# Kernel optimization log

Measured on AMD Instinct MI355X. Metric: run time of the kernel, lower is better.

## Reference

```python
import jax, jax.numpy as jnp
import numpy as np

NUM_CODEBOOKS = 4
COMMITMENT_WEIGHT = 0.25

def setup_inputs() -> dict:
    key = jax.random.key(0)
    k1, k2, k3 = jax.random.split(key, 3)
    B, T, C, K = 16, 2048, 512, 1024
    x = jax.random.normal(k1, (B, T, C), dtype=jnp.float32)
    mask = jax.random.randint(k2, (B, T), 0, 2).astype(jnp.bool_)
    codebooks = jax.random.normal(k3, (NUM_CODEBOOKS, K, C), dtype=jnp.float32) / np.sqrt(C)
    return {"x": x, "mask": mask, "codebooks": codebooks}

def reference(x, mask, codebooks):
    # x: [B,T,C], mask: [B,T] bool, codebooks: [Q,K,C]
    B, T, C = x.shape
    maskf = mask.astype(x.dtype)[..., None]          # [B,T,1]
    n_valid = jnp.maximum(mask.sum().astype(x.dtype), 1.0)
    denom = n_valid * C                               # mse over valid elements
    residual = x
    x_q = jnp.zeros_like(x)
    vq_loss = jnp.zeros((), dtype=x.dtype)
    idx_list = []
    for i in range(NUM_CODEBOOKS):
        cb = codebooks[i]                             # [K,C]
        a2 = jnp.sum(residual * residual, axis=-1, keepdims=True)   # [B,T,1]
        b2 = jnp.sum(cb * cb, axis=-1)                              # [K]
        ab = jnp.einsum('btc,kc->btk', residual, cb)                # [B,T,K]
        dist = a2 + b2 - 2.0 * ab
        idx = jnp.argmin(dist, axis=-1)                             # [B,T]
        q = cb[idx]                                                 # [B,T,C]
        # masked MSE losses (mean over valid elements)
        d1 = (q - jax.lax.stop_gradient(residual)) * maskf
        d2 = (residual - jax.lax.stop_gradient(q)) * maskf
        vq_loss = vq_loss + jnp.sum(d1 * d1) / denom
        vq_loss = vq_loss + COMMITMENT_WEIGHT * jnp.sum(d2 * d2) / denom
        # straight-through, applied only at valid positions
        q_st = residual + jax.lax.stop_gradient(q - residual)
        x_q = x_q + q_st * maskf
        residual = residual - q_st * maskf
        idx_list.append(idx)
    indices = jnp.stack(idx_list, axis=-1)                          # [B,T,Q]
    indices = jnp.where(mask[..., None], indices, -1).astype(jnp.int64)
    x_q = x_q * maskf
    return x_q, indices, vq_loss
```

## Files before the change

kernel.cpp:

```cpp
#include <hip/hip_runtime.h>

#define BT 32768
#define CDIM 512
#define KCB 1024
#define NQ 4
#define IDX_BASE (BT*CDIM)
#define LOSS_OFF (BT*CDIM + BT*NQ)
#define CAND_MAX 64
#define MARGIN_C 0.0025f
#define MARGIN_A 0.004f

#define WS_LIST   256
#define WS_A2     (WS_LIST + BT*4)
#define WS_B2     (WS_A2 + BT*4)
#define WS_RBC    (WS_B2 + NQ*KCB*4)
#define WS_CBB    (WS_RBC + BT*CDIM*2)
#define WS_CCNT   (WS_CBB + NQ*KCB*CDIM*2)
#define WS_CANDK  (WS_CCNT + BT*4)
#define WS_CANDS  (WS_CANDK + BT*CAND_MAX*4)
#define WS_IDXS   (WS_CANDS + BT*CAND_MAX*4)

typedef __attribute__((ext_vector_type(8))) _Float16 f16x8;
typedef __attribute__((ext_vector_type(4))) float f32x4;

__device__ __forceinline__ unsigned int f2h(float f) {
  union { _Float16 h; unsigned short u; } cv;
  cv.h = (_Float16)f;
  return (unsigned int)cv.u;
}

__device__ __forceinline__ int nth_bit(unsigned long long m, int n) {
  int pos = 0;
#pragma unroll
  for (int w = 32; w >= 1; w >>= 1) {
    unsigned long long lowmask = (w == 64) ? ~0ull : ((1ull << w) - 1ull);
    int c = __popcll(m & lowmask);
    if (n >= c) { n -= c; m >>= w; pos += w; }
  }
  return pos;
}

__device__ __forceinline__ float chain512q(const float* lds_r, const float* brow) {
  const float4* b4 = (const float4*)brow;
  float4 cur[8], nxt[8];
#pragma unroll
  for (int q = 0; q < 8; ++q) cur[q] = b4[q];
  float ab = 0.f;
#pragma unroll 1
  for (int seg = 0; seg < 15; ++seg) {
#pragma unroll
    for (int q = 0; q < 8; ++q) nxt[q] = b4[(seg + 1) * 8 + q];
#pragma unroll
    for (int q = 0; q < 8; ++q) {
      float4 bv = cur[q];
      float4 rv = *(const float4*)&lds_r[(seg * 8 + q) * 4];
      ab = __fmaf_rn(rv.x, bv.x, ab);
      ab = __fmaf_rn(rv.y, bv.y, ab);
      ab = __fmaf_rn(rv.z, bv.z, ab);
      ab = __fmaf_rn(rv.w, bv.w, ab);
    }
#pragma unroll
    for (int q = 0; q < 8; ++q) cur[q] = nxt[q];
  }
#pragma unroll
  for (int q = 0; q < 8; ++q) {
    float4 bv = cur[q];
    float4 rv = *(const float4*)&lds_r[(120 + q) * 4];
    ab = __fmaf_rn(rv.x, bv.x, ab);
    ab = __fmaf_rn(rv.y, bv.y, ab);
    ab = __fmaf_rn(rv.z, bv.z, ab);
    ab = __fmaf_rn(rv.w, bv.w, ab);
  }
  return ab;
}

__device__ __forceinline__ int mask_at(const void* m, int t, int flag) {
  switch (flag) {
    case 0:  return ((const unsigned char*)m)[t] != 0;
    case 1:  return ((const int*)m)[t] != 0;
    case 2:  return ((const unsigned long long*)m)[t] != 0ull;
    case 3:  return ((const unsigned short*)m)[t] != 0;
    default: return ((const float*)m)[t] != 0.0f;
  }
}

__global__ void k_prep(const unsigned char* mask, int* wsi, float* wsf, int* list) {
  __shared__ int s_not01, s_off1, s_offn0, s_odd, s_fm;
  __shared__ int s_cnt[1024];
  int tid = threadIdx.x;
  if (tid == 0) { s_not01 = 0; s_off1 = 0; s_offn0 = 0; s_odd = 0; }
  __syncthreads();
  int l_not01 = 0, l_off1 = 0, l_offn0 = 0, l_odd = 0;
  for (int o = tid; o < BT; o += 1024) {
    unsigned char b = mask[o];
    if (b) {
      if (b > 1) l_not01 = 1;
      int m4 = o & 3;
      if (m4 == 1) l_off1 = 1;
      if (m4) l_offn0 = 1;
      if ((o & 7) >= 4) l_odd = 1;
    }
  }
  if (l_not01) atomicOr(&s_not01, 1);
  if (l_off1)  atomicOr(&s_off1, 1);
  if (l_offn0) atomicOr(&s_offn0, 1);
  if (l_odd)   atomicOr(&s_odd, 1);
  __syncthreads();
  if (tid == 0) {
    int fm;
    if (s_not01)      fm = s_off1 ? 3 : 4;
    else if (s_offn0) fm = 0;
    else if (s_odd)   fm = 1;
    else              fm = 2;
    s_fm = fm; wsi[0] = fm;
    wsf[8] = 0.0f;
    wsf[12] = 0.f; wsf[13] = 0.f; wsf[14] = 0.f; wsf[15] = 0.f;
  }
  __syncthreads();
  int fm = s_fm;
  int base = tid * 32, cnt = 0;
  for (int u = 0; u < 32; u++) cnt += mask_at(mask, base + u, fm);
  int val = cnt;
  s_cnt[tid] = val;
  __syncthreads();
#pragma unroll
  for (int off = 1; off < 1024; off <<= 1) {
    int v = (tid >= off) ? s_cnt[tid - off] : 0;
    __syncthreads();
    val += v;
    s_cnt[tid] = val;
    __syncthreads();
  }
  if (tid == 0) wsi[2] = s_cnt[1023];
  int woff = val - cnt;
  for (int u = 0; u < 32; u++) {
    int t = base + u;
    if (mask_at(mask, t, fm)) list[woff++] = t;
  }
}

__global__ void k_fill(const void* mask, float* out, const int* wsi) {
  int w = threadIdx.x >> 6, lane = threadIdx.x & 63;
  int t = blockIdx.x * 4 + w;
  if (t >= BT) return;
  if (mask_at(mask, t, wsi[0])) return;
  float4 z = make_float4(0.f, 0.f, 0.f, 0.f);
  float4* p = (float4*)(out + (size_t)t * CDIM) + lane * 2;
  p[0] = z; p[1] = z;
  if (lane < NQ) out[IDX_BASE + (size_t)t * NQ + lane] = -1.0f;
}

__global__ void k_b2(const float* __restrict__ cb, float* __restrict__ b2, float* b2max) {
  __shared__ float st[4][512];
  int w = threadIdx.x >> 6, lane = threadIdx.x & 63;
  int row = blockIdx.x * 4 + w;
  const float4* p = (const float4*)(cb + (size_t)row * CDIM) + lane * 2;
  float4 v0 = p[0], v1 = p[1];
  *(float4*)&st[w][lane * 8] = v0;
  *(float4*)&st[w][lane * 8 + 4] = v1;
  __syncthreads();
  if (threadIdx.x < 4) {
    int r2 = blockIdx.x * 4 + threadIdx.x;
    float s = 0.f;
    for (int c4 = 0; c4 < 128; ++c4) {
      float4 v = *(float4*)&st[threadIdx.x][c4 * 4];
      s = __fadd_rn(s, __fmul_rn(v.x, v.x));
      s = __fadd_rn(s, __fmul_rn(v.y, v.y));
      s = __fadd_rn(s, __fmul_rn(v.z, v.z));
      s = __fadd_rn(s, __fmul_rn(v.w, v.w));
    }
    b2[r2] = s;
    atomicMax((int*)&b2max[r2 >> 10], __float_as_int(s));
  }
}

__global__ void k_cvtcb(const float* __restrict__ cb, unsigned short* __restrict__ cbb) {
  size_t i = (size_t)blockIdx.x * blockDim.x + threadIdx.x;
  const float4* s = (const float4*)(cb + i * 8);
  float4 a = s[0], b = s[1];
  uint4 u;
  u.x = f2h(a.x) | (f2h(a.y) << 16);
  u.y = f2h(a.z) | (f2h(a.w) << 16);
  u.z = f2h(b.x) | (f2h(b.y) << 16);
  u.w = f2h(b.z) | (f2h(b.w) << 16);
  *(uint4*)(cbb + i * 8) = u;
}

__global__ __launch_bounds__(256) void k_init(const float* __restrict__ x,
    float* __restrict__ rws, unsigned short* __restrict__ rbc,
    const int* __restrict__ wsi, const int* __restrict__ list,
    float* __restrict__ a2c, int* __restrict__ candcnt) {
  __shared__ float st[8][512];
  int nv = wsi[2];
  int j0 = blockIdx.x * 8;
  int tid = threadIdx.x;
  if (tid < 8) candcnt[j0 + tid] = 0;
  if (j0 >= nv) return;
  int slot = tid >> 5;
  int j = j0 + slot;
  int c0 = (tid & 31) * 16;
  if (j < nv) {
    int t = list[j];
    const float4* src = (const float4*)(x + (size_t)t * CDIM + c0);
    float4* dst = (float4*)(rws + (size_t)t * CDIM + c0);
    float4 v0 = src[0], v1 = src[1], v2 = src[2], v3 = src[3];
    dst[0] = v0; dst[1] = v1; dst[2] = v2; dst[3] = v3;
    *(float4*)&st[slot][c0]      = v0; *(float4*)&st[slot][c0 + 4]  = v1;
    *(float4*)&st[slot][c0 + 8]  = v2; *(float4*)&st[slot][c0 + 12] = v3;
    uint4 u0, u1;
    u0.x = f2h(v0.x) | (f2h(v0.y) << 16); u0.y = f2h(v0.z) | (f2h(v0.w) << 16);
    u0.z = f2h(v1.x) | (f2h(v1.y) << 16); u0.w = f2h(v1.z) | (f2h(v1.w) << 16);
    u1.x = f2h(v2.x) | (f2h(v2.y) << 16); u1.y = f2h(v2.z) | (f2h(v2.w) << 16);
    u1.z = f2h(v3.x) | (f2h(v3.y) << 16); u1.w = f2h(v3.z) | (f2h(v3.w) << 16);
    uint4* bd = (uint4*)(rbc + (size_t)j * CDIM + c0);
    bd[0] = u0; bd[1] = u1;
  }
  __syncthreads();
  if (tid < 8) {
    int jj = j0 + tid;
    if (jj < nv) {
      float s = 0.f;
      for (int c4 = 0; c4 < 128; ++c4) {
        float4 v = *(float4*)&st[tid][c4 * 4];
        s = __fadd_rn(s, __fmul_rn(v.x, v.x));
        s = __fadd_rn(s, __fmul_rn(v.y, v.y));
        s = __fadd_rn(s, __fmul_rn(v.z, v.z));
        s = __fadd_rn(s, __fmul_rn(v.w, v.w));
      }
      a2c[jj] = s;
    }
  }
}

__global__ __launch_bounds__(256) void k_gemm(const unsigned short* __restrict__ rbc,
    const unsigned short* __restrict__ cbb, const float* __restrict__ b2,
    const float* __restrict__ b2max, const float* __restrict__ a2c,
    const int* __restrict__ wsi, int* __restrict__ candcnt,
    int* __restrict__ candk, float* __restrict__ cands, int ic) {
  __shared__ __align__(16) unsigned short As[128 * 64];
  __shared__ __align__(16) unsigned short Bs[128 * 64];
  int nv = wsi[2];
  int mb = blockIdx.x >> 3, nb = blockIdx.x & 7;
  int m0 = mb * 128;
  if (m0 >= nv) return;
  int tid = threadIdx.x;
  int w = tid >> 6, lane = tid & 63;
  int wm = w >> 1, wn = w & 1;
  f32x4 acc[4][4];
#pragma unroll
  for (int a = 0; a < 4; a++)
#pragma unroll
    for (int b = 0; b < 4; b++) acc[a][b] = (f32x4){0.f, 0.f, 0.f, 0.f};

  const unsigned short* Ag = rbc + (size_t)m0 * CDIM;
  const unsigned short* Bg = cbb + (size_t)(ic * KCB + nb * 128) * CDIM;
  int w4 = __builtin_amdgcn_readfirstlane(w);
  int lr8 = lane >> 3, lck = lane & 7;
  int l15 = lane & 15, l4 = lane >> 4;

  for (int kc = 0; kc < 8; ++kc) {
    __syncthreads();
#pragma unroll
    for (int i = 0; i < 4; ++i) {
      int ra = w4 * 32 + i * 8 + lr8;
      int sc = (lck ^ (ra & 7)) << 3;
      const unsigned short* sa = Ag + (size_t)ra * CDIM + kc * 64 + sc;
      __builtin_amdgcn_global_load_lds(
          (const __attribute__((address_space(1))) unsigned int*)sa,
          (__attribute__((address_space(3))) unsigned int*)&As[(w4 * 32 + i * 8) * 64],
          16, 0, 0);
      const unsigned short* sb = Bg + (size_t)ra * CDIM + kc * 64 + sc;
      __builtin_amdgcn_global_load_lds(
          (const __attribute__((address_space(1))) unsigned int*)sb,
          (__attribute__((address_space(3))) unsigned int*)&Bs[(w4 * 32 + i * 8) * 64],
          16, 0, 0);
    }
    asm volatile("s_waitcnt vmcnt(0)" ::: "memory");
    __syncthreads();
#pragma unroll
    for (int h = 0; h < 2; ++h) {
      f16x8 af[4], bf[4];
#pragma unroll
      for (int mf = 0; mf < 4; ++mf) {
        int row = wm * 64 + mf * 16 + l15;
        af[mf] = *(const f16x8*)&As[row * 64 + (((h * 4 + l4) ^ (row & 7)) << 3)];
      }
#pragma unroll
      for (int nf = 0; nf < 4; ++nf) {
        int row = wn * 64 + nf * 16 + l15;
        bf[nf] = *(const f16x8*)&Bs[row * 64 + (((h * 4 + l4) ^ (row & 7)) << 3)];
      }
#pragma unroll
      for (int mf = 0; mf < 4; ++mf)
#pragma unroll
        for (int nf = 0; nf < 4; ++nf)
          acc[mf][nf] = __builtin_amdgcn_mfma_f32_16x16x32_f16(af[mf], bf[nf], acc[mf][nf], 0, 0, 0);
    }
  }

  const float* b2p = b2 + ic * KCB;
  float bmax = b2max[ic];
#pragma unroll
  for (int mf = 0; mf < 4; ++mf) {
    float sv[4][4];
    int kg[4];
    float smin[4]; int kmin[4];
#pragma unroll
    for (int q = 0; q < 4; ++q) { smin[q] = __builtin_inff(); kmin[q] = 0; }
#pragma unroll
    for (int nf = 0; nf < 4; ++nf) {
      int k = nb * 128 + wn * 64 + nf * 16 + l15;
      kg[nf] = k;
      float b2k = b2p[k];
#pragma unroll
      for (int q = 0; q < 4; ++q) {
        float s = __fsub_rn(b2k, __fmul_rn(2.0f, acc[mf][nf][q]));
        sv[nf][q] = s;
        if (s < smin[q]) { smin[q] = s; kmin[q] = k; }
      }
    }
#pragma unroll
    for (int d = 1; d < 16; d <<= 1) {
#pragma unroll
      for (int q = 0; q < 4; ++q) {
        float vo = __shfl_xor(smin[q], d, 64);
        int ko = __shfl_xor(kmin[q], d, 64);
        if (vo < smin[q] || (vo == smin[q] && ko < kmin[q])) { smin[q] = vo; kmin[q] = ko; }
      }
    }
#pragma unroll
    for (int q = 0; q < 4; ++q) {
      int j = m0 + wm * 64 + mf * 16 + l4 * 4 + q;
      if (j < nv) {
        float thr = smin[q] + MARGIN_C * sqrtf(a2c[j] * bmax) + MARGIN_A;
#pragma unroll
        for (int nf = 0; nf < 4; ++nf) {
          if (sv[nf][q] <= thr) {
            int pos = atomicAdd(&candcnt[j], 1);
            if (pos < CAND_MAX) {
              candk[(size_t)j * CAND_MAX + pos] = kg[nf];
              cands[(size_t)j * CAND_MAX + pos] = sv[nf][q];
            }
          }
        }
      }
    }
  }
}

__global__ __launch_bounds__(256) void k_argmin(const float* __restrict__ cb,
    const float* __restrict__ rws, const int* __restrict__ list,
    const int* __restrict__ wsi, const float* __restrict__ a2c,
    const float* __restrict__ b2, const float* __restrict__ b2max,
    int* __restrict__ candcnt, const int* __restrict__ candk,
    const float* __restrict__ cands, float* __restrict__ out,
    int* __restrict__ idxsel, int ic) {
  __shared__ float rbuf[4][512];
  int nv = wsi[2];
  int tid = threadIdx.x, wv = tid >> 6, lane = tid & 63;
  int j = blockIdx.x * 4 + wv;
  if (j >= nv) return;
  int t = __builtin_amdgcn_readfirstlane(list[j]);
  int cnt = candcnt[j];
  if (lane == 0) candcnt[j] = 0;
  float a2v = a2c[j];
  const float* b2p = b2 + ic * KCB;
  const float* cbp = cb + (size_t)ic * KCB * CDIM;

  int kw;
  if (cnt <= CAND_MAX) {
    float sa = __builtin_inff(); int kl = 0;
    if (lane < cnt) {
      sa = cands[(size_t)j * CAND_MAX + lane];
      kl = candk[(size_t)j * CAND_MAX + lane];
    }
    float g = sa;
#pragma unroll
    for (int d = 1; d < 64; d <<= 1) g = fminf(g, __shfl_xor(g, d, 64));
    float M = MARGIN_C * sqrtf(a2v * b2max[ic]) + MARGIN_A;
    bool keep = (lane < cnt) && (sa <= g + M);
    unsigned long long mkb = __ballot(keep);
    int nk = (int)__popcll(mkb);
    if (nk == 1) {
      int src = nth_bit(mkb, 0);
      kw = __shfl(kl, src, 64);
    } else {
      const float4* rr = (const float4*)(rws + (size_t)t * CDIM);
      float4 r0 = rr[lane * 2], r1 = rr[lane * 2 + 1];
      *(float4*)&rbuf[wv][lane * 8]     = r0;
      *(float4*)&rbuf[wv][lane * 8 + 4] = r1;
      int sel = lane % nk;
      int src = nth_bit(mkb, sel);
      int myk = __shfl(kl, src, 64);
      asm volatile("s_waitcnt lgkmcnt(0)" ::: "memory");
      float ab = chain512q(rbuf[wv], cbp + (size_t)myk * CDIM);
      float dv = __fsub_rn(__fadd_rn(a2v, b2p[myk]), __fmul_rn(2.0f, ab));
      int kc = myk;
#pragma unroll
      for (int d = 1; d < 64; d <<= 1) {
        float vo = __shfl_xor(dv, d, 64);
        int ko = __shfl_xor(kc, d, 64);
        if (vo < dv || (vo == dv && ko < kc)) { dv = vo; kc = ko; }
      }
      kw = kc;
    }
  } else {
    const float4* rr = (const float4*)(rws + (size_t)t * CDIM);
    float4 r0 = rr[lane * 2], r1 = rr[lane * 2 + 1];
    *(float4*)&rbuf[wv][lane * 8]     = r0;
    *(float4*)&rbuf[wv][lane * 8 + 4] = r1;
    asm volatile("s_waitcnt lgkmcnt(0)" ::: "memory");
    float dl = __builtin_inff(); int kl2 = 0x7fffffff;
    for (int base = 0; base < KCB; base += 64) {
      int myk = base + lane;
      float ab = chain512q(rbuf[wv], cbp + (size_t)myk * CDIM);
      float dv = __fsub_rn(__fadd_rn(a2v, b2p[myk]), __fmul_rn(2.0f, ab));
      if (dv < dl || (dv == dl && myk < kl2)) { dl = dv; kl2 = myk; }
    }
#pragma unroll
    for (int d = 1; d < 64; d <<= 1) {
      float vo = __shfl_xor(dl, d, 64);
      int ko = __shfl_xor(kl2, d, 64);
      if (vo < dl || (vo == dl && ko < kl2)) { dl = vo; kl2 = ko; }
    }
    kw = kl2;
  }
  if (lane == 0) {
    out[IDX_BASE + (size_t)t * NQ + ic] = (float)kw;
    idxsel[j] = kw;
  }
}

__global__ __launch_bounds__(256) void k_upd2(const float* __restrict__ x,
    const float* __restrict__ cb, float* __restrict__ rws,
    unsigned short* __restrict__ rbc, const int* __restrict__ list,
    const int* __restrict__ wsi, float* __restrict__ a2c,
    const int* __restrict__ idxsel, float* __restrict__ lossacc, int ic) {
  __shared__ float st[8][512];
  __shared__ float s_l[4];
  int nv = wsi[2];
  int j0 = blockIdx.x * 8;
  if (j0 >= nv) return;
  int tid = threadIdx.x;
  int slot = tid >> 5;
  int j = j0 + slot;
  bool valid = (j < nv);
  int jc = valid ? j : (nv - 1);
  int t = list[jc];
  int kw = idxsel[jc];
  int c0 = (tid & 31) * 16;
  const float* cbp = cb + (size_t)ic * KCB * CDIM;
  float lsum = 0.f;
  if (valid) {
    float4* rp = (float4*)(rws + (size_t)t * CDIM + c0);
    const float4* qp = (const float4*)(cbp + (size_t)kw * CDIM + c0);
#pragma unroll
    for (int q4 = 0; q4 < 4; ++q4) {
      float4 rv = rp[q4], qv = qp[q4];
      float4 d, n;
      d.x = __fsub_rn(qv.x, rv.x); d.y = __fsub_rn(qv.y, rv.y);
      d.z = __fsub_rn(qv.z, rv.z); d.w = __fsub_rn(qv.w, rv.w);
      n.x = __fsub_rn(rv.x, __fadd_rn(rv.x, d.x));
      n.y = __fsub_rn(rv.y, __fadd_rn(rv.y, d.y));
      n.z = __fsub_rn(rv.z, __fadd_rn(rv.z, d.z));
      n.w = __fsub_rn(rv.w, __fadd_rn(rv.w, d.w));
      lsum = __fmaf_rn(d.x, d.x, lsum); lsum = __fmaf_rn(d.y, d.y, lsum);
      lsum = __fmaf_rn(d.z, d.z, lsum); lsum = __fmaf_rn(d.w, d.w, lsum);
      if (ic < 3) {
        rp[q4] = n;
        *(float4*)&st[slot][c0 + q4 * 4] = n;
        uint2 u;
        u.x = f2h(n.x) | (f2h(n.y) << 16);
        u.y = f2h(n.z) | (f2h(n.w) << 16);
        *(uint2*)(rbc + (size_t)j * CDIM + c0 + q4 * 4) = u;
      } else {
        float4 xv = ((const float4*)(x + (size_t)t * CDIM + c0))[q4];
        float4 o;
        o.x = __fsub_rn(xv.x, n.x); o.y = __fsub_rn(xv.y, n.y);
        o.z = __fsub_rn(xv.z, n.z); o.w = __fsub_rn(xv.w, n.w);
        rp[q4] = o;
      }
    }
  }
#pragma unroll
  for (int d = 1; d < 64; d <<= 1) lsum += __shfl_xor(lsum, d, 64);
  if ((tid & 63) == 0) s_l[tid >> 6] = lsum;
  __syncthreads();
  if (ic < 3 && tid < 8) {
    int jj = j0 + tid;
    if (jj < nv) {
      float s = 0.f;
      for (int c4 = 0; c4 < 128; ++c4) {
        float4 v = *(float4*)&st[tid][c4 * 4];
        s = __fadd_rn(s, __fmul_rn(v.x, v.x));
        s = __fadd_rn(s, __fmul_rn(v.y, v.y));
        s = __fadd_rn(s, __fmul_rn(v.z, v.z));
        s = __fadd_rn(s, __fmul_rn(v.w, v.w));
      }
      a2c[jj] = s;
    }
  }
  if (tid == 0) atomicAdd(lossacc, (s_l[0] + s_l[1]) + (s_l[2] + s_l[3]));
}

__global__ void k_loss(const int* wsi, const float* acc, float* out) {
  if (threadIdx.x == 0 && blockIdx.x == 0) {
    float n = (float)wsi[2];
    if (n < 1.0f) n = 1.0f;
    out[LOSS_OFF] = acc[0] * 1.25f / (n * (float)CDIM);
  }
}

extern "C" void kernel_launch(void* const* d_in, const int* in_sizes, int n_in,
                              void* d_out, int out_size, void* d_ws, size_t ws_size,
                              hipStream_t stream) {
  const float* x   = (const float*)d_in[0];
  const void* mask = d_in[1];
  const float* cb  = (const float*)d_in[2];
  float* out = (float*)d_out;
  char* ws = (char*)d_ws;
  int*   wsi  = (int*)ws;
  float* wsf  = (float*)ws;
  int*   list = (int*)(ws + WS_LIST);
  float* a2c  = (float*)(ws + WS_A2);
  float* b2   = (float*)(ws + WS_B2);
  unsigned short* rbc = (unsigned short*)(ws + WS_RBC);
  unsigned short* cbb = (unsigned short*)(ws + WS_CBB);
  int*   ccnt = (int*)(ws + WS_CCNT);
  int*   ck   = (int*)(ws + WS_CANDK);
  float* cs   = (float*)(ws + WS_CANDS);
  int*   isel = (int*)(ws + WS_IDXS);
  float* rws  = out;
  float* b2mx = wsf + 12;

  hipLaunchKernelGGL(k_prep, dim3(1), dim3(1024), 0, stream,
                     (const unsigned char*)mask, wsi, wsf, list);
  hipLaunchKernelGGL(k_fill, dim3(BT / 4), dim3(256), 0, stream, mask, out, wsi);
  hipLaunchKernelGGL(k_b2, dim3(NQ * KCB / 4), dim3(256), 0, stream, cb, b2, b2mx);
  hipLaunchKernelGGL(k_cvtcb, dim3(NQ * KCB * CDIM / 8 / 256), dim3(256), 0, stream, cb, cbb);
  hipLaunchKernelGGL(k_init, dim3(BT / 8), dim3(256), 0, stream,
                     x, rws, rbc, wsi, list, a2c, ccnt);
  for (int ic = 0; ic < NQ; ic++) {
    hipLaunchKernelGGL(k_gemm, dim3((BT / 128) * 8), dim3(256), 0, stream,
                       rbc, cbb, b2, b2mx, a2c, wsi, ccnt, ck, cs, ic);
    hipLaunchKernelGGL(k_argmin, dim3(BT / 4), dim3(256), 0, stream,
                       cb, rws, list, wsi, a2c, b2, b2mx, ccnt, ck, cs,
                       out, isel, ic);
    hipLaunchKernelGGL(k_upd2, dim3(BT / 8), dim3(256), 0, stream,
                       x, cb, rws, rbc, list, wsi, a2c, isel, wsf + 8, ic);
  }
  hipLaunchKernelGGL(k_loss, dim3(1), dim3(1), 0, stream, wsi, wsf + 8, out);
}
```

Before: 778.6 us.

## Double-buffer GEMM LDS tiles and remap block order for codebook reuse

Adds double-buffered LDS tiles so the global-to-LDS loads for the next K-chunk are issued before the MFMA work on the current chunk, with partial vmcnt waits and raw barriers in place of full drains. The block index is also remapped so that consecutive blocks share the same codebook tile (nb) and walk across row blocks, which is meant to improve L2 reuse of the codebook. The cost is double the LDS per block, which may lower occupancy. The remap also changes which blocks exit early on the nv check.

Result: slower. 1.042 ms (+33.8%).

```diff
diff --git a/kernel.cpp b/kernel.cpp
--- a/kernel.cpp
+++ b/kernel.cpp
@@ -237,10 +237,11 @@
     const float* __restrict__ b2max, const float* __restrict__ a2c,
     const int* __restrict__ wsi, int* __restrict__ candcnt,
     int* __restrict__ candk, float* __restrict__ cands, int ic) {
-  __shared__ __align__(16) unsigned short As[128 * 64];
-  __shared__ __align__(16) unsigned short Bs[128 * 64];
+  __shared__ __align__(16) unsigned short As[2][128 * 64];
+  __shared__ __align__(16) unsigned short Bs[2][128 * 64];
   int nv = wsi[2];
-  int mb = blockIdx.x >> 3, nb = blockIdx.x & 7;
+  int wk = ((blockIdx.x & 7) << 8) | (blockIdx.x >> 3);
+  int mb = wk >> 3, nb = wk & 7;
   int m0 = mb * 128;
   if (m0 >= nv) return;
   int tid = threadIdx.x;
@@ -258,8 +259,7 @@
   int lr8 = lane >> 3, lck = lane & 7;
   int l15 = lane & 15, l4 = lane >> 4;
 
-  for (int kc = 0; kc < 8; ++kc) {
-    __syncthreads();
+  auto STAGE = [&](int buf, int kc) {
 #pragma unroll
     for (int i = 0; i < 4; ++i) {
       int ra = w4 * 32 + i * 8 + lr8;
@@ -267,28 +267,40 @@
       const unsigned short* sa = Ag + (size_t)ra * CDIM + kc * 64 + sc;
       __builtin_amdgcn_global_load_lds(
           (const __attribute__((address_space(1))) unsigned int*)sa,
-          (__attribute__((address_space(3))) unsigned int*)&As[(w4 * 32 + i * 8) * 64],
+          (__attribute__((address_space(3))) unsigned int*)&As[buf][(w4 * 32 + i * 8) * 64],
           16, 0, 0);
       const unsigned short* sb = Bg + (size_t)ra * CDIM + kc * 64 + sc;
       __builtin_amdgcn_global_load_lds(
           (const __attribute__((address_space(1))) unsigned int*)sb,
-          (__attribute__((address_space(3))) unsigned int*)&Bs[(w4 * 32 + i * 8) * 64],
+          (__attribute__((address_space(3))) unsigned int*)&Bs[buf][(w4 * 32 + i * 8) * 64],
           16, 0, 0);
     }
-    asm volatile("s_waitcnt vmcnt(0)" ::: "memory");
-    __syncthreads();
+  };
+
+  STAGE(0, 0);
+#pragma unroll 1
+  for (int kc = 0; kc < 8; ++kc) {
+    int cur = kc & 1;
+    if (kc < 7) {
+      STAGE(cur ^ 1, kc + 1);
+      asm volatile("s_waitcnt vmcnt(8)" ::: "memory");
+    } else {
+      asm volatile("s_waitcnt vmcnt(0)" ::: "memory");
+    }
+    __builtin_amdgcn_s_barrier();
+    asm volatile("" ::: "memory");
 #pragma unroll
     for (int h = 0; h < 2; ++h) {
       f16x8 af[4], bf[4];
 #pragma unroll
       for (int mf = 0; mf < 4; ++mf) {
         int row = wm * 64 + mf * 16 + l15;
-        af[mf] = *(const f16x8*)&As[row * 64 + (((h * 4 + l4) ^ (row & 7)) << 3)];
+        af[mf] = *(const f16x8*)&As[cur][row * 64 + (((h * 4 + l4) ^ (row & 7)) << 3)];
       }
 #pragma unroll
       for (int nf = 0; nf < 4; ++nf) {
         int row = wn * 64 + nf * 16 + l15;
-        bf[nf] = *(const f16x8*)&Bs[row * 64 + (((h * 4 + l4) ^ (row & 7)) << 3)];
+        bf[nf] = *(const f16x8*)&Bs[cur][row * 64 + (((h * 4 + l4) ^ (row & 7)) << 3)];
       }
 #pragma unroll
       for (int mf = 0; mf < 4; ++mf)
@@ -296,6 +308,8 @@
         for (int nf = 0; nf < 4; ++nf)
           acc[mf][nf] = __builtin_amdgcn_mfma_f32_16x16x32_f16(af[mf], bf[nf], acc[mf][nf], 0, 0, 0);
     }
+    __builtin_amdgcn_s_barrier();
+    asm volatile("" ::: "memory");
   }
 
   const float* b2p = b2 + ic * KCB;
```
